# Kernel optimization log

Measured on AMD Instinct MI355X. Metric: run time of the kernel, lower is better.

## Reference

```python
import jax, jax.numpy as jnp
import numpy as np

BLOCK = 64  # NF4 block size
SCALING = 32.0 / 16.0  # lora_alpha / r

# Standard NF4 (normal-float 4-bit) codebook, 16 levels
NF4_TABLE = jnp.asarray([
    -1.0, -0.6961928009986877, -0.5250730514526367, -0.39491748809814453,
    -0.28444138169288635, -0.18477343022823334, -0.09105003625154495, 0.0,
    0.07958029955625534, 0.16093020141124725, 0.24611230194568634,
    0.33791524171829224, 0.44070982933044434, 0.5626170039176941,
    0.7229568362236023, 1.0], dtype=jnp.float32)


def dequant_nf4(codes, scales):
    # codes: [out, in] int in [0,16); scales: [out, in//BLOCK] float
    out_f, in_f = codes.shape
    w = NF4_TABLE[codes].reshape(out_f, in_f // BLOCK, BLOCK)
    w = w * scales[:, :, None]
    return w.reshape(out_f, in_f)


def setup_inputs() -> dict:
    key = jax.random.key(0)
    k1, k2, k3, k4, k5 = jax.random.split(key, 5)
    B, S, D_in, D_out, R = 4, 2048, 4096, 4096, 16
    x = jax.random.normal(k1, (B, S, D_in), dtype=jnp.float32)
    codes = jax.random.randint(k2, (D_out, D_in), 0, 16, dtype=jnp.int32)
    scales = jax.random.uniform(k3, (D_out, D_in // BLOCK), dtype=jnp.float32)
    lora_A = jax.random.normal(k4, (R, D_in), dtype=jnp.float32) * (1.0 / np.sqrt(D_in))
    lora_B = jax.random.normal(k5, (D_out, R), dtype=jnp.float32) * 0.02
    return {"x": x, "codes": codes, "scales": scales,
            "lora_A": lora_A, "lora_B": lora_B}


def reference(x, codes, scales, lora_A, lora_B):
    # Base path: F.linear(x, dequant(W))  -> x @ W^T
    W = dequant_nf4(codes, scales)            # [out, in]
    base = jnp.einsum('bsd,od->bso', x, W)    # [B, S, out]
    # LoRA path (dropout p=0.0 -> identity): (x @ A^T) @ B^T * scaling
    lora = jnp.einsum('bsr,or->bso', jnp.einsum('bsd,rd->bsr', x, lora_A), lora_B)
    return base + lora * SCALING
```

## Files before the change

### kernel.cpp

```cpp
#include <hip/hip_runtime.h>
#include <hip/hip_bf16.h>

typedef __attribute__((ext_vector_type(8))) short short8;
typedef __attribute__((ext_vector_type(4))) short short4v;
typedef __attribute__((ext_vector_type(4))) float floatx4;

#define M_DIM 8192
#define N_DIM 4096
#define K_DIM 4096
#define BM 128
#define BN 128
#define BK 64

__device__ __constant__ float NF4_TAB[16] = {
    -1.0f, -0.6961928009986877f, -0.5250730514526367f, -0.39491748809814453f,
    -0.28444138169288635f, -0.18477343022823334f, -0.09105003625154495f, 0.0f,
    0.07958029955625534f, 0.16093020141124725f, 0.24611230194568634f,
    0.33791524171829224f, 0.44070982933044434f, 0.5626170039176941f,
    0.7229568362236023f, 1.0f};

__global__ __launch_bounds__(256)
void dequant_lora_kernel(const int* __restrict__ codes,
                         const float* __restrict__ scales,
                         const float* __restrict__ la,
                         const float* __restrict__ lb,
                         short4v* __restrict__ W) {
    __shared__ float tab[16];
    if (threadIdx.x < 16) tab[threadIdx.x] = NF4_TAB[threadIdx.x];
    __syncthreads();

    const int kb = blockIdx.x & 3;
    const int n0 = (blockIdx.x >> 2) << 4;
    const int k0 = kb * 1024 + threadIdx.x * 4;

    float4 a[16];
#pragma unroll
    for (int r = 0; r < 16; r++)
        a[r] = *(const float4*)(la + (size_t)r * K_DIM + k0);

#pragma unroll 4
    for (int i = 0; i < 16; i++) {
        const int n = n0 + i;
        int4 c = *(const int4*)(codes + (size_t)n * K_DIM + k0);
        float s = scales[(n << 6) + (k0 >> 6)];
        const float* bp = lb + (n << 4);
        float acc0 = 0.f, acc1 = 0.f, acc2 = 0.f, acc3 = 0.f;
#pragma unroll
        for (int r = 0; r < 16; r++) {
            float br = bp[r];
            acc0 += br * a[r].x;
            acc1 += br * a[r].y;
            acc2 += br * a[r].z;
            acc3 += br * a[r].w;
        }
        union { short4v v; __hip_bfloat16 h[4]; } u;
        u.h[0] = __float2bfloat16(tab[c.x] * s + 2.0f * acc0);
        u.h[1] = __float2bfloat16(tab[c.y] * s + 2.0f * acc1);
        u.h[2] = __float2bfloat16(tab[c.z] * s + 2.0f * acc2);
        u.h[3] = __float2bfloat16(tab[c.w] * s + 2.0f * acc3);
        W[((size_t)n * K_DIM + k0) >> 2] = u.v;
    }
}

__global__ void cast_x_kernel(const float* __restrict__ x,
                              short8* __restrict__ xb) {
    int g = blockIdx.x * blockDim.x + threadIdx.x;
    const float4* xp = (const float4*)(x + (size_t)g * 8);
    float4 v0 = xp[0], v1 = xp[1];
    union { short8 v; __hip_bfloat16 h[8]; } u;
    u.h[0] = __float2bfloat16(v0.x);
    u.h[1] = __float2bfloat16(v0.y);
    u.h[2] = __float2bfloat16(v0.z);
    u.h[3] = __float2bfloat16(v0.w);
    u.h[4] = __float2bfloat16(v1.x);
    u.h[5] = __float2bfloat16(v1.y);
    u.h[6] = __float2bfloat16(v1.z);
    u.h[7] = __float2bfloat16(v1.w);
    xb[g] = u.v;
}

#define GL2LDS(gsrc, ldst)                                                   \
    __builtin_amdgcn_global_load_lds(                                        \
        (const __attribute__((address_space(1))) void*)(gsrc),               \
        (__attribute__((address_space(3))) void*)(ldst), 16, 0, 0)

__global__ __launch_bounds__(256, 3)
void gemm_bt_kernel(const __hip_bfloat16* __restrict__ A,
                    const __hip_bfloat16* __restrict__ B,
                    float* __restrict__ C) {
    __shared__ __align__(16) __hip_bfloat16 sA[BM * BK];
    __shared__ __align__(16) __hip_bfloat16 sB[BN * BK];
    const int tid = threadIdx.x;
    const int wave = tid >> 6;
    const int lane = tid & 63;
    const int q = lane >> 4;
    const int t = lane & 15;
    const int wm = wave >> 1;
    const int wn = wave & 1;
    const int bm0 = blockIdx.y * BM;
    const int bn0 = blockIdx.x * BN;

    floatx4 acc[4][4] = {};

    const __hip_bfloat16* ga[4];
    const __hip_bfloat16* gb[4];
#pragma unroll
    for (int i = 0; i < 4; i++) {
        int rt = i * 32 + (tid >> 3);
        int cb = (tid & 7) ^ (rt & 7);
        ga[i] = A + (size_t)(bm0 + rt) * K_DIM + cb * 8;
        gb[i] = B + (size_t)(bn0 + rt) * K_DIM + cb * 8;
    }

    for (int k0 = 0; k0 < K_DIM; k0 += BK) {
#pragma unroll
        for (int i = 0; i < 4; i++) {
            GL2LDS(ga[i] + k0, (char*)sA + (i * 256 + wave * 64) * 16);
            GL2LDS(gb[i] + k0, (char*)sB + (i * 256 + wave * 64) * 16);
        }
        __syncthreads();
#pragma unroll
        for (int ks = 0; ks < BK; ks += 32) {
            short8 af[4], bfr[4];
#pragma unroll
            for (int mi = 0; mi < 4; mi++) {
                int row = wm * 64 + mi * 16 + t;
                int cb = (ks >> 3) + q;
                af[mi] = *(const short8*)&sA[row * 64 + ((cb ^ (row & 7)) << 3)];
            }
#pragma unroll
            for (int ni = 0; ni < 4; ni++) {
                int row = wn * 64 + ni * 16 + t;
                int cb = (ks >> 3) + q;
                bfr[ni] = *(const short8*)&sB[row * 64 + ((cb ^ (row & 7)) << 3)];
            }
#pragma unroll
            for (int mi = 0; mi < 4; mi++)
#pragma unroll
                for (int ni = 0; ni < 4; ni++)
                    acc[mi][ni] = __builtin_amdgcn_mfma_f32_16x16x32_bf16(
                        af[mi], bfr[ni], acc[mi][ni], 0, 0, 0);
        }
        __syncthreads();
    }

#pragma unroll
    for (int mi = 0; mi < 4; mi++) {
        int row0 = bm0 + wm * 64 + mi * 16 + q * 4;
#pragma unroll
        for (int ni = 0; ni < 4; ni++) {
            int col = bn0 + wn * 64 + ni * 16 + t;
            float* cp = C + (size_t)row0 * N_DIM + col;
#pragma unroll
            for (int r = 0; r < 4; r++) cp[(size_t)r * N_DIM] = acc[mi][ni][r];
        }
    }
}

extern "C" void kernel_launch(void* const* d_in, const int* in_sizes, int n_in,
                              void* d_out, int out_size, void* d_ws,
                              size_t ws_size, hipStream_t stream) {
    const float* x = (const float*)d_in[0];
    const int* codes = (const int*)d_in[1];
    const float* scales = (const float*)d_in[2];
    const float* loraA = (const float*)d_in[3];
    const float* loraB = (const float*)d_in[4];
    float* out = (float*)d_out;

    char* ws = (char*)d_ws;
    __hip_bfloat16* xb = (__hip_bfloat16*)ws;
    __hip_bfloat16* Wb = (__hip_bfloat16*)(ws + 67108864);

    dequant_lora_kernel<<<dim3(4 * (N_DIM / 16)), dim3(256), 0, stream>>>(
        codes, scales, loraA, loraB, (short4v*)Wb);
    cast_x_kernel<<<dim3((M_DIM * (K_DIM / 8)) / 256), dim3(256), 0, stream>>>(
        x, (short8*)xb);
    gemm_bt_kernel<<<dim3(N_DIM / BN, M_DIM / BM), dim3(256), 0, stream>>>(
        xb, Wb, out);
}
```

Before: 523.6 us.

## Rewrite GEMM as 256x256 tile, 8-wave, double-buffered pipelined kernel

```diff
diff --git a/kernel.cpp b/kernel.cpp
--- a/kernel.cpp
+++ b/kernel.cpp
@@ -8,8 +8,6 @@
 #define M_DIM 8192
 #define N_DIM 4096
 #define K_DIM 4096
-#define BM 128
-#define BN 128
 #define BK 64
 
 __device__ __constant__ float NF4_TAB[16] = {
@@ -84,72 +82,146 @@
         (const __attribute__((address_space(1))) void*)(gsrc),               \
         (__attribute__((address_space(3))) void*)(ldst), 16, 0, 0)
 
-__global__ __launch_bounds__(256, 3)
+
+#define STAGE_A(D, H, T) do {                                                 \
+    GL2LDS(gA0 + (size_t)((H) * 128) * K_DIM + (T) * BK,                      \
+           ldsA + (D) * 32768 + (H) * 16384 + ldsw);                          \
+    GL2LDS(gA0 + (size_t)((H) * 128 + 64) * K_DIM + (T) * BK,                 \
+           ldsA + (D) * 32768 + (H) * 16384 + 8192 + ldsw);                   \
+} while (0)
+
+#define STAGE_B(D, H, T) do {                                                 \
+    GL2LDS(gB0 + (size_t)((H) * 128) * K_DIM + (T) * BK,                      \
+           ldsB + (D) * 32768 + (H) * 16384 + ldsw);                          \
+    GL2LDS(gB0 + (size_t)((H) * 128 + 64) * K_DIM + (T) * BK,                 \
+           ldsB + (D) * 32768 + (H) * 16384 + 8192 + ldsw);                   \
+} while (0)
+
+#define MFMA_Q(AF, BF, MB, NB) do {                                           \
+    _Pragma("unroll") for (int mi_ = 0; mi_ < 4; mi_++)                       \
+    _Pragma("unroll") for (int ni_ = 0; ni_ < 2; ni_++)                       \
+    _Pragma("unroll") for (int ks_ = 0; ks_ < 2; ks_++)                       \
+        acc[(MB) + mi_][(NB) + ni_] =                                         \
+            __builtin_amdgcn_mfma_f32_16x16x32_bf16(                          \
+                AF[mi_][ks_], BF[ni_][ks_], acc[(MB) + mi_][(NB) + ni_],      \
+                0, 0, 0);                                                     \
+} while (0)
+
+#define LGKM0 asm volatile("s_waitcnt lgkmcnt(0)" ::: "memory")
+#define VM4   asm volatile("s_waitcnt vmcnt(4)" ::: "memory")
+#define VM0   asm volatile("s_waitcnt vmcnt(0)" ::: "memory")
+#define VMNONE do {} while (0)
+
+#define TILE(T, D, DOB, DOA, VM) do {                                         \
+    short8 af0[4][2], af1[4][2], bf0[2][2], bf1[2][2];                        \
+                                 \
+    _Pragma("unroll") for (int mi_ = 0; mi_ < 4; mi_++) {                     \
+        int o_ = (D) * 32768 + aoff + mi_ * 2048;                             \
+        af0[mi_][0] = *(const short8*)(ldsA + o_);                            \
+        af0[mi_][1] = *(const short8*)(ldsA + (o_ ^ 64));                     \
+    }                                                                         \
+    _Pragma("unroll") for (int ni_ = 0; ni_ < 2; ni_++) {                     \
+        int o_ = (D) * 32768 + boff + ni_ * 2048;                             \
+        bf0[ni_][0] = *(const short8*)(ldsB + o_);                            \
+        bf0[ni_][1] = *(const short8*)(ldsB + (o_ ^ 64));                     \
+    }                                                                         \
+    if (DOB) STAGE_B((D) ^ 1, 0, (T) + 1);                                    \
+    __builtin_amdgcn_s_barrier();                                             \
+    LGKM0;                                                                    \
+    __builtin_amdgcn_s_setprio(1);                                            \
+    MFMA_Q(af0, bf0, 0, 0);                                                   \
+    __builtin_amdgcn_s_setprio(0);                                            \
+    __builtin_amdgcn_s_barrier();                                             \
+                                          \
+    _Pragma("unroll") for (int mi_ = 0; mi_ < 4; mi_++) {                     \
+        int o_ = (D) * 32768 + aoff + 8192 + mi_ * 2048;                      \
+        af1[mi_][0] = *(const short8*)(ldsA + o_);                            \
+        af1[mi_][1] = *(const short8*)(ldsA + (o_ ^ 64));                     \
+    }                                                                         \
+    if (DOB) STAGE_B((D) ^ 1, 1, (T) + 1);                                    \
+    __builtin_amdgcn_s_barrier();                                             \
+    LGKM0;                                                                    \
+    __builtin_amdgcn_s_setprio(1);                                            \
+    MFMA_Q(af1, bf0, 4, 0);                                                   \
+    __builtin_amdgcn_s_setprio(0);                                            \
+    __builtin_amdgcn_s_barrier();                                             \
+                                          \
+    _Pragma("unroll") for (int ni_ = 0; ni_ < 2; ni_++) {                     \
+        int o_ = (D) * 32768 + boff + 4096 + ni_ * 2048;                      \
+        bf1[ni_][0] = *(const short8*)(ldsB + o_);                            \
+        bf1[ni_][1] = *(const short8*)(ldsB + (o_ ^ 64));                     \
+    }                                                                         \
+    if (DOA) STAGE_A((D), 0, (T) + 2);                                        \
+    __builtin_amdgcn_s_barrier();                                             \
+    LGKM0;                                                                    \
+    __builtin_amdgcn_s_setprio(1);                                            \
+    MFMA_Q(af0, bf1, 0, 2);                                                   \
+    __builtin_amdgcn_s_setprio(0);                                            \
+    __builtin_amdgcn_s_barrier();                                             \
+                       \
+    if (DOA) STAGE_A((D), 1, (T) + 2);                                        \
+    VM;                                                                       \
+    __builtin_amdgcn_s_barrier();                                             \
+    __builtin_amdgcn_s_setprio(1);                                            \
+    MFMA_Q(af1, bf1, 4, 2);                                                   \
+    __builtin_amdgcn_s_setprio(0);                                            \
+    __builtin_amdgcn_s_barrier();                                             \
+} while (0)
+
+__global__ __launch_bounds__(512, 2)
 void gemm_bt_kernel(const __hip_bfloat16* __restrict__ A,
                     const __hip_bfloat16* __restrict__ B,
                     float* __restrict__ C) {
-    __shared__ __align__(16) __hip_bfloat16 sA[BM * BK];
-    __shared__ __align__(16) __hip_bfloat16 sB[BN * BK];
+    __shared__ __align__(16) char lds[131072];
+    char* ldsA = (char*)lds;
+    char* ldsB = (char*)lds + 65536;
+
     const int tid = threadIdx.x;
     const int wave = tid >> 6;
     const int lane = tid & 63;
     const int q = lane >> 4;
-    const int t = lane & 15;
-    const int wm = wave >> 1;
-    const int wn = wave & 1;
-    const int bm0 = blockIdx.y * BM;
-    const int bn0 = blockIdx.x * BN;
-
-    floatx4 acc[4][4] = {};
-
-    const __hip_bfloat16* ga[4];
-    const __hip_bfloat16* gb[4];
-#pragma unroll
-    for (int i = 0; i < 4; i++) {
-        int rt = i * 32 + (tid >> 3);
-        int cb = (tid & 7) ^ (rt & 7);
-        ga[i] = A + (size_t)(bm0 + rt) * K_DIM + cb * 8;
-        gb[i] = B + (size_t)(bn0 + rt) * K_DIM + cb * 8;
+    const int t16 = lane & 15;
+    const int wm = wave >> 2;
+    const int wn = wave & 3;
+
+    const int bid = blockIdx.x;
+    const int swz = ((bid & 7) << 6) | (bid >> 3);
+    const int bm0 = (swz >> 4) << 8;
+    const int bn0 = (swz & 15) << 8;
+
+    const int sw = (q ^ (t16 & 7)) << 4;
+    const int aoff = (wm * 128 + t16) * 128 + sw;
+    const int boff = (wn * 64 + t16) * 128 + sw;
+
+    const int r0 = tid >> 3;
+    const int c0 = ((tid & 7) ^ (r0 & 7)) << 3;
+    const __hip_bfloat16* gA0 = A + (size_t)(bm0 + r0) * K_DIM + c0;
+    const __hip_bfloat16* gB0 = B + (size_t)(bn0 + r0) * K_DIM + c0;
+    const int ldsw = wave << 10;
+
+    floatx4 acc[8][4] = {};
+
+    STAGE_A(0, 0, 0); STAGE_A(0, 1, 0);
+    STAGE_B(0, 0, 0); STAGE_B(0, 1, 0);
+    STAGE_A(1, 0, 1); STAGE_A(1, 1, 1);
+    VM4;
+    __builtin_amdgcn_s_barrier();
+
+#pragma unroll 1
+    for (int tp = 0; tp < 31; ++tp) {
+        const int t2 = tp << 1;
+        TILE(t2, 0, 1, 1, VM4);
+        TILE(t2 + 1, 1, 1, 1, VM4);
     }
-
-    for (int k0 = 0; k0 < K_DIM; k0 += BK) {
-#pragma unroll
-        for (int i = 0; i < 4; i++) {
-            GL2LDS(ga[i] + k0, (char*)sA + (i * 256 + wave * 64) * 16);
-            GL2LDS(gb[i] + k0, (char*)sB + (i * 256 + wave * 64) * 16);
-        }
-        __syncthreads();
-#pragma unroll
-        for (int ks = 0; ks < BK; ks += 32) {
-            short8 af[4], bfr[4];
-#pragma unroll
-            for (int mi = 0; mi < 4; mi++) {
-                int row = wm * 64 + mi * 16 + t;
-                int cb = (ks >> 3) + q;
-                af[mi] = *(const short8*)&sA[row * 64 + ((cb ^ (row & 7)) << 3)];
-            }
-#pragma unroll
-            for (int ni = 0; ni < 4; ni++) {
-                int row = wn * 64 + ni * 16 + t;
-                int cb = (ks >> 3) + q;
-                bfr[ni] = *(const short8*)&sB[row * 64 + ((cb ^ (row & 7)) << 3)];
-            }
-#pragma unroll
-            for (int mi = 0; mi < 4; mi++)
-#pragma unroll
-                for (int ni = 0; ni < 4; ni++)
-                    acc[mi][ni] = __builtin_amdgcn_mfma_f32_16x16x32_bf16(
-                        af[mi], bfr[ni], acc[mi][ni], 0, 0, 0);
-        }
-        __syncthreads();
-    }
-
-#pragma unroll
-    for (int mi = 0; mi < 4; mi++) {
-        int row0 = bm0 + wm * 64 + mi * 16 + q * 4;
+    TILE(62, 0, 1, 0, VM0);
+    TILE(63, 1, 0, 0, VMNONE);
+
+#pragma unroll
+    for (int mi = 0; mi < 8; mi++) {
+        int row0 = bm0 + wm * 128 + mi * 16 + q * 4;
 #pragma unroll
         for (int ni = 0; ni < 4; ni++) {
-            int col = bn0 + wn * 64 + ni * 16 + t;
+            int col = bn0 + wn * 64 + ni * 16 + t16;
             float* cp = C + (size_t)row0 * N_DIM + col;
 #pragma unroll
             for (int r = 0; r < 4; r++) cp[(size_t)r * N_DIM] = acc[mi][ni][r];
@@ -175,6 +247,5 @@
         codes, scales, loraA, loraB, (short4v*)Wb);
     cast_x_kernel<<<dim3((M_DIM * (K_DIM / 8)) / 256), dim3(256), 0, stream>>>(
         x, (short8*)xb);
-    gemm_bt_kernel<<<dim3(N_DIM / BN, M_DIM / BM), dim3(256), 0, stream>>>(
-        xb, Wb, out);
-}
+    gemm_bt_kernel<<<dim3(512), dim3(512), 0, stream>>>(xb, Wb, out);
+}
```

Measured after the change: 483.6 us. 1.08x faster.
